# Kernel tuning notes

Measured on AMD Instinct MI355X. Metric: run time of the kernel, lower is better.

Reference implementation:

```python
import jax, jax.numpy as jnp
import numpy as np

NUM_TILES = 64
TPC = 8            # tiles per cluster
GRID = 16          # spline grid size
EPS = 1e-5


def setup_inputs() -> dict:
    key = jax.random.key(0)
    ks = jax.random.split(key, 6)
    B, S, D, T, DH, G = 2, 1024, 512, NUM_TILES, 128, GRID
    x = jax.random.normal(ks[0], (B, S, D), dtype=jnp.float32)
    gamma = jnp.ones((D,), jnp.float32)
    beta = jnp.zeros((D,), jnp.float32)
    # torch layouts: down.weight [DH, D], up.weight [D, DH]
    Wd = jax.random.normal(ks[1], (T, DH, D), dtype=jnp.float32) * 0.02
    spline_bases = jax.random.normal(ks[2], (T, DH, G), dtype=jnp.float32) * 0.1
    spline_slopes = jax.random.normal(ks[3], (T, DH, G), dtype=jnp.float32) * 0.1
    Wu = jax.random.normal(ks[4], (T, D, DH), dtype=jnp.float32) * 0.02
    scale = jnp.full((T,), 0.1, jnp.float32)
    return {"x": x, "gamma": gamma, "beta": beta, "Wd": Wd,
            "spline_bases": spline_bases, "spline_slopes": spline_slopes,
            "Wu": Wu, "scale": scale}


def reference(x, gamma, beta, Wd, spline_bases, spline_slopes, Wu, scale):
    B, S, D = x.shape
    T, DH, _ = Wd.shape
    C = T // TPC
    N = B * S

    # LayerNorm
    mu = x.mean(-1, keepdims=True)
    var = ((x - mu) ** 2).mean(-1, keepdims=True)
    xn = (x - mu) * jax.lax.rsqrt(var + EPS) * gamma + beta
    xf = xn.reshape(N, D)

    # Signatures (first call: ema == current tile signatures)
    tile_sigs = jnp.sign(Wd.mean(axis=1))                         # [T, D]
    cluster_sigs = jnp.sign(tile_sigs.reshape(C, TPC, D).mean(1))  # [C, D]

    # Hierarchical routing: cluster -> tile
    in_sigs = jnp.sign(xf)                                        # [N, D]
    best_c = jnp.argmax(in_sigs @ cluster_sigs.T, axis=-1)        # [N]
    tile_scores = (in_sigs @ tile_sigs.T).reshape(N, C, TPC)      # [N, C, TPC]
    sc = jnp.take_along_axis(tile_scores, best_c[:, None, None], axis=1)[:, 0, :]
    local_best = jnp.argmax(sc, axis=-1)                          # [N]
    tidx = best_c * TPC + local_best                              # [N]

    # Dispatch: gather per-token expert weights, down-project
    h = jnp.einsum('nd,nhd->nh', xf, Wd[tidx])                    # [N, DH]

    # Spline nonlinearity
    hn = jax.nn.sigmoid(h)
    idx = jnp.clip((hn * GRID).astype(jnp.int32), 0, GRID - 1)    # [N, DH]
    base = jnp.take_along_axis(spline_bases[tidx], idx[..., None], axis=-1)[..., 0]
    slope = jnp.take_along_axis(spline_slopes[tidx], idx[..., None], axis=-1)[..., 0]
    local_pos = hn * GRID - idx.astype(h.dtype)                   # (hn - idx*cell)/cell
    hs = base + slope * local_pos                                 # [N, DH]

    # Up-project, per-tile scale, combine (dropout is identity in eval)
    y = jnp.einsum('nh,ndh->nd', hs, Wu[tidx]) * scale[tidx][:, None]
    return x + y.reshape(B, S, D)
```

## Files before the change

### kernel.cpp

```cpp
#include <hip/hip_runtime.h>
#include <hip/hip_bf16.h>
#include <math.h>

#define NTILES 64
#define TPC 8
#define NCLUST 8
#define GRID_SZ 16
#define DIM 512
#define DHID 128
#define NTOK 2048
#define LN_EPS 1e-5f
#define TB 16
#define NCHUNK_MAX 192

typedef __attribute__((ext_vector_type(8))) short bf16x8;
typedef __attribute__((ext_vector_type(4))) float f32x4;
typedef unsigned long long u64;

static __device__ __forceinline__ unsigned short bf16bits(float f) {
    union { __hip_bfloat16 h; unsigned short s; } u;
    u.h = __float2bfloat16(f);
    return u.s;
}

static __device__ __forceinline__ bf16x8 cvt8v(float4 a, float4 b) {
    float e[8] = {a.x, a.y, a.z, a.w, b.x, b.y, b.z, b.w};
    bf16x8 v;
    #pragma unroll
    for (int i = 0; i < 8; ++i) v[i] = (short)bf16bits(e[i]);
    return v;
}

static __device__ __forceinline__ bf16x8 cvt8(const float* p) {
    return cvt8v(*(const float4*)p, *(const float4*)(p + 4));
}

static __device__ __forceinline__ u64 maj3(u64 a, u64 b, u64 c) {
    return (a & b) | (c & (a ^ b));
}

static __device__ __forceinline__ bool route_chunk(const int* counts, int lane, int cb,
                                                   int& t, int& base, int& m) {
    int cnt_l = counts[lane];
    int nck = (cnt_l + TB - 1) / TB;
    int pre = nck;
    #pragma unroll
    for (int off = 1; off < 64; off <<= 1) {
        int u = __shfl_up(pre, off);
        if (lane >= off) pre += u;
    }
    int total = __shfl(pre, 63);
    pre -= nck;
    if (cb >= total) return false;
    u64 msk = __ballot(cb >= pre && cb < pre + nck);
    t = (int)__builtin_ctzll(msk);
    base = (cb - __shfl(pre, t)) * TB;
    m = min(TB, __shfl(cnt_l, t) - base);
    return true;
}

__global__ __launch_bounds__(512) void k_prep(const float* __restrict__ x,
                                              const float* __restrict__ gamma,
                                              const float* __restrict__ beta,
                                              const float* __restrict__ Wd,
                                              unsigned short* __restrict__ wd_b,
                                              unsigned short* __restrict__ xn_b,
                                              u64* __restrict__ tbits,
                                              int* __restrict__ counts) {
    int bid = blockIdx.x;
    int tid = threadIdx.x;
    int lane = tid & 63;
    int wv = tid >> 6;
    if (bid < NTILES) {
        int t = bid;
        if (bid == 0 && tid < NTILES) counts[tid] = 0;
        const float* bp = Wd + (size_t)t * DHID * DIM + tid;
        unsigned short* bb = wd_b + (size_t)t * DHID * DIM + tid;
        float s0 = 0.f, s1 = 0.f, s2 = 0.f, s3 = 0.f;
        #pragma unroll 4
        for (int j = 0; j < DHID; j += 4) {
            float v0 = bp[(size_t)(j + 0) * DIM];
            float v1 = bp[(size_t)(j + 1) * DIM];
            float v2 = bp[(size_t)(j + 2) * DIM];
            float v3 = bp[(size_t)(j + 3) * DIM];
            bb[(size_t)(j + 0) * DIM] = bf16bits(v0);
            bb[(size_t)(j + 1) * DIM] = bf16bits(v1);
            bb[(size_t)(j + 2) * DIM] = bf16bits(v2);
            bb[(size_t)(j + 3) * DIM] = bf16bits(v3);
            s0 += v0; s1 += v1; s2 += v2; s3 += v3;
        }
        float s = (s0 + s1) + (s2 + s3);
        u64 b = __ballot(s < 0.f);
        if (lane == 0) tbits[t * 8 + wv] = b;
    } else {
        int n = (bid - NTILES) * 8 + wv;
        const float* xr = x + (size_t)n * DIM;
        float v[8];
        float sum = 0.f;
        #pragma unroll
        for (int j = 0; j < 8; ++j) { float t = xr[lane + 64 * j]; v[j] = t; sum += t; }
        #pragma unroll
        for (int off = 32; off; off >>= 1) sum += __shfl_xor(sum, off);
        float mu = sum * (1.f / DIM);
        float sq = 0.f;
        #pragma unroll
        for (int j = 0; j < 8; ++j) { float t = v[j] - mu; sq += t * t; }
        #pragma unroll
        for (int off = 32; off; off >>= 1) sq += __shfl_xor(sq, off);
        float rs = rsqrtf(sq * (1.f / DIM) + LN_EPS);
        #pragma unroll
        for (int j = 0; j < 8; ++j) {
            int d = lane + 64 * j;
            float xv = (v[j] - mu) * rs * gamma[d] + beta[d];
            xn_b[(size_t)n * DIM + d] = bf16bits(xv);
        }
    }
}

__global__ __launch_bounds__(256) void k_route(const unsigned short* __restrict__ xn_b,
                                               const u64* __restrict__ tbits,
                                               int* __restrict__ counts,
                                               int* __restrict__ list) {
    int n = blockIdx.x * 4 + (threadIdx.x >> 6);
    int lane = threadIdx.x & 63;
    u64 xb[8];
    #pragma unroll
    for (int j = 0; j < 8; ++j) {
        unsigned short u = xn_b[(size_t)n * DIM + lane + 64 * j];
        xb[j] = __ballot((u & 0x8000u) != 0 && (u & 0x7fffu) != 0);
    }
    const u64* tb = tbits + lane * 8;
    int ts = 0;
    #pragma unroll
    for (int j = 0; j < 8; ++j) ts += __popcll(xb[j] ^ tb[j]);
    int tscore = DIM - 2 * ts;

    int c = lane >> 3, jw = lane & 7;
    u64 x0 = tbits[(c * TPC + 0) * 8 + jw], x1 = tbits[(c * TPC + 1) * 8 + jw];
    u64 x2 = tbits[(c * TPC + 2) * 8 + jw], x3 = tbits[(c * TPC + 3) * 8 + jw];
    u64 x4 = tbits[(c * TPC + 4) * 8 + jw], x5 = tbits[(c * TPC + 5) * 8 + jw];
    u64 x6 = tbits[(c * TPC + 6) * 8 + jw], x7 = tbits[(c * TPC + 7) * 8 + jw];
    u64 s0 = x0 ^ x1 ^ x2, c0 = maj3(x0, x1, x2);
    u64 s1 = x3 ^ x4 ^ x5, c1 = maj3(x3, x4, x5);
    u64 s2 = x6 ^ x7,      c2 = x6 & x7;
    u64 t0 = s0 ^ s1 ^ s2, t1 = maj3(s0, s1, s2);
    u64 p = c0 ^ c1, q = c0 & c1;
    u64 r = c2 ^ t1, s_ = c2 & t1;
    u64 S0 = p ^ r, car = p & r;
    u64 W0 = (q ^ s_) ^ car;
    u64 W1 = (q & s_) | (car & (q ^ s_));
    u64 cbit = W1 | (W0 & (S0 | t0));
    u64 cmsk = ~(W0 & ~W1 & ~S0 & ~t0);
    int ps = __popcll(cmsk) - 2 * __popcll((xb[jw] ^ cbit) & cmsk);
    ps += __shfl_xor(ps, 1);
    ps += __shfl_xor(ps, 2);
    ps += __shfl_xor(ps, 4);

    int bc = 0, best = __shfl(ps, 0);
    #pragma unroll
    for (int k = 1; k < NCLUST; ++k) {
        int v = __shfl(ps, k * 8);
        if (v > best) { best = v; bc = k; }
    }
    int bt = bc * TPC, bts = __shfl(tscore, bc * TPC);
    #pragma unroll
    for (int k = 1; k < TPC; ++k) {
        int v = __shfl(tscore, bc * TPC + k);
        if (v > bts) { bts = v; bt = bc * TPC + k; }
    }
    if (lane == 0) {
        int slot = atomicAdd(&counts[bt], 1);
        list[(size_t)bt * NTOK + slot] = n;
    }
}

__global__ __launch_bounds__(512, 2) void k_ffn(const float* __restrict__ x,
                                                const unsigned short* __restrict__ xn_b,
                                                const unsigned short* __restrict__ wd_b,
                                                const float* __restrict__ sb,
                                                const float* __restrict__ ss,
                                                const float* __restrict__ Wu,
                                                const float* __restrict__ scale,
                                                const int* __restrict__ counts,
                                                const int* __restrict__ list,
                                                float* __restrict__ out) {
    int tid = threadIdx.x;
    int lane = tid & 63;
    int wv = tid >> 6;
    int cb = ((int)blockIdx.x & 7) * (NCHUNK_MAX / 8) + ((int)blockIdx.x >> 3);
    int t, base, m;
    if (!route_chunk(counts, lane, cb, t, base, m)) return;

    __shared__ __align__(16) unsigned short hsl[TB * DHID];

    int mrow = lane & 15;
    int ko = (lane >> 4) * 8;
    int tokm = list[(size_t)t * NTOK + base + min(mrow, m - 1)];

    const unsigned short* xr = xn_b + (size_t)tokm * DIM;
    const unsigned short* wr = wd_b + ((size_t)t * DHID + wv * 16 + mrow) * DIM;
    f32x4 acc0 = {0.f, 0.f, 0.f, 0.f}, acc1 = acc0;
    #pragma unroll
    for (int kk = 0; kk < 8; ++kk) {
        int d0 = kk * 32 + ko;
        int d1 = (kk + 8) * 32 + ko;
        bf16x8 a0 = *(const bf16x8*)(xr + d0);
        bf16x8 b0 = *(const bf16x8*)(wr + d0);
        acc0 = __builtin_amdgcn_mfma_f32_16x16x32_bf16(a0, b0, acc0, 0, 0, 0);
        bf16x8 a1 = *(const bf16x8*)(xr + d1);
        bf16x8 b1 = *(const bf16x8*)(wr + d1);
        acc1 = __builtin_amdgcn_mfma_f32_16x16x32_bf16(a1, b1, acc1, 0, 0, 0);
    }
    f32x4 acc = acc0 + acc1;

    const float* wru0 = Wu + ((size_t)t * DIM + wv * 64 + mrow) * DHID;
    float4 pfa[4], pfb[4];
    #pragma unroll
    for (int kk = 0; kk < 4; ++kk) {
        pfa[kk] = *(const float4*)(wru0 + kk * 32 + ko);
        pfb[kk] = *(const float4*)(wru0 + kk * 32 + ko + 4);
    }

    int dh = wv * 16 + mrow;
    const float* sbt = sb + ((size_t)t * DHID + dh) * GRID_SZ;
    const float* sst = ss + ((size_t)t * DHID + dh) * GRID_SZ;
    #pragma unroll
    for (int r = 0; r < 4; ++r) {
        int tr = (lane >> 4) * 4 + r;
        float h = acc[r];
        float hn = 1.f / (1.f + expf(-h));
        float g = hn * (float)GRID_SZ;
        int idx = (int)g;
        idx = idx > GRID_SZ - 1 ? GRID_SZ - 1 : idx;
        float lp = g - (float)idx;
        float val = sbt[idx] + sst[idx] * lp;
        hsl[(tr * DHID + dh) ^ ((tr & 7) << 3)] = bf16bits(val);
    }
    __syncthreads();

    float sc_t = scale[t];
    bf16x8 a2[4];
    #pragma unroll
    for (int kk = 0; kk < 4; ++kk)
        a2[kk] = *(const bf16x8*)&hsl[(mrow * DHID + kk * 32 + ko) ^ ((mrow & 7) << 3)];
    #pragma unroll
    for (int nt = 0; nt < 4; ++nt) {
        int d = wv * 64 + nt * 16 + mrow;
        const float* wru = Wu + ((size_t)t * DIM + d) * DHID;
        f32x4 au = {0.f, 0.f, 0.f, 0.f};
        #pragma unroll
        for (int kk = 0; kk < 4; ++kk) {
            bf16x8 b = (nt == 0) ? cvt8v(pfa[kk], pfb[kk])
                                 : cvt8(wru + kk * 32 + ko);
            au = __builtin_amdgcn_mfma_f32_16x16x32_bf16(a2[kk], b, au, 0, 0, 0);
        }
        #pragma unroll
        for (int r = 0; r < 4; ++r) {
            int tr = (lane >> 4) * 4 + r;
            int tok_tr = __shfl(tokm, tr);
            if (tr < m) {
                size_t o = (size_t)tok_tr * DIM + d;
                out[o] = x[o] + au[r] * sc_t;
            }
        }
    }
}

extern "C" void kernel_launch(void* const* d_in, const int* in_sizes, int n_in,
                              void* d_out, int out_size, void* d_ws, size_t ws_size,
                              hipStream_t stream) {
    const float* x     = (const float*)d_in[0];
    const float* gamma = (const float*)d_in[1];
    const float* beta  = (const float*)d_in[2];
    const float* Wd    = (const float*)d_in[3];
    const float* sb    = (const float*)d_in[4];
    const float* ss    = (const float*)d_in[5];
    const float* Wu    = (const float*)d_in[6];
    const float* scale = (const float*)d_in[7];
    float* out = (float*)d_out;

    u64*   tbits         = (u64*)d_ws;
    int*   counts        = (int*)(tbits + NTILES * 8);
    int*   list          = counts + NTILES;
    unsigned short* xn_b = (unsigned short*)(list + (size_t)NTILES * NTOK);
    unsigned short* wd_b = xn_b + (size_t)NTOK * DIM;

    k_prep<<<NTILES + NTOK / 8, 512, 0, stream>>>(x, gamma, beta, Wd, wd_b, xn_b, tbits, counts);
    k_route<<<NTOK / 4, 256, 0, stream>>>(xn_b, tbits, counts, list);
    k_ffn<<<NCHUNK_MAX, 512, 0, stream>>>(x, xn_b, wd_b, sb, ss, Wu, scale, counts, list, out);
}
```

Measured before the change: 50.49 us.

## Pre-convert Wu to bf16 in prep kernel and prefetch all FFN operands into registers

The prep kernel gains 256 extra blocks that convert Wu to bf16 in workspace, and the Wd conversion now uses float4 loads with a shared-memory reduction for the sign sums. The FFN kernel loads all down-projection operands and all bf16 up-projection weights into registers up front instead of interleaving loads with MFMAs and converting fp32 Wu per chunk. This halves Wu bytes read in the FFN and removes repeated per-chunk conversion. In exchange, the prep kernel writes a full bf16 copy of Wu, and register pressure rises, so launch bounds drop to one block per CU.

```diff
diff --git a/kernel.cpp b/kernel.cpp
--- a/kernel.cpp
+++ b/kernel.cpp
@@ -14,6 +14,7 @@
 #define NCHUNK_MAX 192
 
 typedef __attribute__((ext_vector_type(8))) short bf16x8;
+typedef __attribute__((ext_vector_type(4))) unsigned short u16x4;
 typedef __attribute__((ext_vector_type(4))) float f32x4;
 typedef unsigned long long u64;
 
@@ -23,16 +24,14 @@
     return u.s;
 }
 
-static __device__ __forceinline__ bf16x8 cvt8v(float4 a, float4 b) {
+static __device__ __forceinline__ bf16x8 cvt8(const float* p) {
+    float4 a = *(const float4*)p;
+    float4 b = *(const float4*)(p + 4);
     float e[8] = {a.x, a.y, a.z, a.w, b.x, b.y, b.z, b.w};
     bf16x8 v;
     #pragma unroll
     for (int i = 0; i < 8; ++i) v[i] = (short)bf16bits(e[i]);
     return v;
-}
-
-static __device__ __forceinline__ bf16x8 cvt8(const float* p) {
-    return cvt8v(*(const float4*)p, *(const float4*)(p + 4));
 }
 
 static __device__ __forceinline__ u64 maj3(u64 a, u64 b, u64 c) {
@@ -63,7 +62,9 @@
                                               const float* __restrict__ gamma,
                                               const float* __restrict__ beta,
                                               const float* __restrict__ Wd,
+                                              const float* __restrict__ Wu,
                                               unsigned short* __restrict__ wd_b,
+                                              unsigned short* __restrict__ wu_b,
                                               unsigned short* __restrict__ xn_b,
                                               u64* __restrict__ tbits,
                                               int* __restrict__ counts) {
@@ -74,25 +75,25 @@
     if (bid < NTILES) {
         int t = bid;
         if (bid == 0 && tid < NTILES) counts[tid] = 0;
-        const float* bp = Wd + (size_t)t * DHID * DIM + tid;
-        unsigned short* bb = wd_b + (size_t)t * DHID * DIM + tid;
-        float s0 = 0.f, s1 = 0.f, s2 = 0.f, s3 = 0.f;
-        #pragma unroll 4
-        for (int j = 0; j < DHID; j += 4) {
-            float v0 = bp[(size_t)(j + 0) * DIM];
-            float v1 = bp[(size_t)(j + 1) * DIM];
-            float v2 = bp[(size_t)(j + 2) * DIM];
-            float v3 = bp[(size_t)(j + 3) * DIM];
-            bb[(size_t)(j + 0) * DIM] = bf16bits(v0);
-            bb[(size_t)(j + 1) * DIM] = bf16bits(v1);
-            bb[(size_t)(j + 2) * DIM] = bf16bits(v2);
-            bb[(size_t)(j + 3) * DIM] = bf16bits(v3);
-            s0 += v0; s1 += v1; s2 += v2; s3 += v3;
-        }
-        float s = (s0 + s1) + (s2 + s3);
+        int q = tid >> 7;
+        int c4 = tid & 127;
+        const float* wp = Wd + ((size_t)t * DHID + q * 32) * DIM + c4 * 4;
+        unsigned short* bp = wd_b + ((size_t)t * DHID + q * 32) * DIM + c4 * 4;
+        float4 a = {0.f, 0.f, 0.f, 0.f};
+        #pragma unroll
+        for (int j = 0; j < 32; ++j) {
+            float4 v = *(const float4*)(wp + (size_t)j * DIM);
+            u16x4 h = {bf16bits(v.x), bf16bits(v.y), bf16bits(v.z), bf16bits(v.w)};
+            *(u16x4*)(bp + (size_t)j * DIM) = h;
+            a.x += v.x; a.y += v.y; a.z += v.z; a.w += v.w;
+        }
+        __shared__ float ps[4][DIM];
+        *(float4*)&ps[q][c4 * 4] = a;
+        __syncthreads();
+        float s = ps[0][tid] + ps[1][tid] + ps[2][tid] + ps[3][tid];
         u64 b = __ballot(s < 0.f);
         if (lane == 0) tbits[t * 8 + wv] = b;
-    } else {
+    } else if (bid < 320) {
         int n = (bid - NTILES) * 8 + wv;
         const float* xr = x + (size_t)n * DIM;
         float v[8];
@@ -113,6 +114,13 @@
             int d = lane + 64 * j;
             float xv = (v[j] - mu) * rs * gamma[d] + beta[d];
             xn_b[(size_t)n * DIM + d] = bf16bits(xv);
+        }
+    } else {
+        size_t basei = (size_t)(bid - 320) * 16384;
+        #pragma unroll
+        for (int k = 0; k < 4; ++k) {
+            size_t off = basei + (size_t)tid * 8 + (size_t)k * 4096;
+            *(bf16x8*)(wu_b + off) = cvt8(Wu + off);
         }
     }
 }
@@ -151,15 +159,15 @@
     u64 W1 = (q & s_) | (car & (q ^ s_));
     u64 cbit = W1 | (W0 & (S0 | t0));
     u64 cmsk = ~(W0 & ~W1 & ~S0 & ~t0);
-    int ps = __popcll(cmsk) - 2 * __popcll((xb[jw] ^ cbit) & cmsk);
-    ps += __shfl_xor(ps, 1);
-    ps += __shfl_xor(ps, 2);
-    ps += __shfl_xor(ps, 4);
-
-    int bc = 0, best = __shfl(ps, 0);
+    int psc = __popcll(cmsk) - 2 * __popcll((xb[jw] ^ cbit) & cmsk);
+    psc += __shfl_xor(psc, 1);
+    psc += __shfl_xor(psc, 2);
+    psc += __shfl_xor(psc, 4);
+
+    int bc = 0, best = __shfl(psc, 0);
     #pragma unroll
     for (int k = 1; k < NCLUST; ++k) {
-        int v = __shfl(ps, k * 8);
+        int v = __shfl(psc, k * 8);
         if (v > best) { best = v; bc = k; }
     }
     int bt = bc * TPC, bts = __shfl(tscore, bc * TPC);
@@ -174,12 +182,12 @@
     }
 }
 
-__global__ __launch_bounds__(512, 2) void k_ffn(const float* __restrict__ x,
+__global__ __launch_bounds__(512, 1) void k_ffn(const float* __restrict__ x,
                                                 const unsigned short* __restrict__ xn_b,
                                                 const unsigned short* __restrict__ wd_b,
                                                 const float* __restrict__ sb,
                                                 const float* __restrict__ ss,
-                                                const float* __restrict__ Wu,
+                                                const unsigned short* __restrict__ wu_b,
                                                 const float* __restrict__ scale,
                                                 const int* __restrict__ counts,
                                                 const int* __restrict__ list,
@@ -199,26 +207,28 @@
 
     const unsigned short* xr = xn_b + (size_t)tokm * DIM;
     const unsigned short* wr = wd_b + ((size_t)t * DHID + wv * 16 + mrow) * DIM;
+    bf16x8 wreg[16], areg[16];
+    #pragma unroll
+    for (int kk = 0; kk < 16; ++kk) {
+        int d = kk * 32 + ko;
+        wreg[kk] = *(const bf16x8*)(wr + d);
+        areg[kk] = *(const bf16x8*)(xr + d);
+    }
     f32x4 acc0 = {0.f, 0.f, 0.f, 0.f}, acc1 = acc0;
     #pragma unroll
     for (int kk = 0; kk < 8; ++kk) {
-        int d0 = kk * 32 + ko;
-        int d1 = (kk + 8) * 32 + ko;
-        bf16x8 a0 = *(const bf16x8*)(xr + d0);
-        bf16x8 b0 = *(const bf16x8*)(wr + d0);
-        acc0 = __builtin_amdgcn_mfma_f32_16x16x32_bf16(a0, b0, acc0, 0, 0, 0);
-        bf16x8 a1 = *(const bf16x8*)(xr + d1);
-        bf16x8 b1 = *(const bf16x8*)(wr + d1);
-        acc1 = __builtin_amdgcn_mfma_f32_16x16x32_bf16(a1, b1, acc1, 0, 0, 0);
+        acc0 = __builtin_amdgcn_mfma_f32_16x16x32_bf16(areg[2 * kk], wreg[2 * kk], acc0, 0, 0, 0);
+        acc1 = __builtin_amdgcn_mfma_f32_16x16x32_bf16(areg[2 * kk + 1], wreg[2 * kk + 1], acc1, 0, 0, 0);
     }
     f32x4 acc = acc0 + acc1;
 
-    const float* wru0 = Wu + ((size_t)t * DIM + wv * 64 + mrow) * DHID;
-    float4 pfa[4], pfb[4];
-    #pragma unroll
-    for (int kk = 0; kk < 4; ++kk) {
-        pfa[kk] = *(const float4*)(wru0 + kk * 32 + ko);
-        pfb[kk] = *(const float4*)(wru0 + kk * 32 + ko + 4);
+    bf16x8 wupf[16];
+    #pragma unroll
+    for (int nt = 0; nt < 4; ++nt) {
+        const unsigned short* wru = wu_b + ((size_t)t * DIM + wv * 64 + nt * 16 + mrow) * DHID;
+        #pragma unroll
+        for (int kk = 0; kk < 4; ++kk)
+            wupf[nt * 4 + kk] = *(const bf16x8*)(wru + kk * 32 + ko);
     }
 
     int dh = wv * 16 + mrow;
@@ -246,14 +256,10 @@
     #pragma unroll
     for (int nt = 0; nt < 4; ++nt) {
         int d = wv * 64 + nt * 16 + mrow;
-        const float* wru = Wu + ((size_t)t * DIM + d) * DHID;
         f32x4 au = {0.f, 0.f, 0.f, 0.f};
         #pragma unroll
-        for (int kk = 0; kk < 4; ++kk) {
-            bf16x8 b = (nt == 0) ? cvt8v(pfa[kk], pfb[kk])
-                                 : cvt8(wru + kk * 32 + ko);
-            au = __builtin_amdgcn_mfma_f32_16x16x32_bf16(a2[kk], b, au, 0, 0, 0);
-        }
+        for (int kk = 0; kk < 4; ++kk)
+            au = __builtin_amdgcn_mfma_f32_16x16x32_bf16(a2[kk], wupf[nt * 4 + kk], au, 0, 0, 0);
         #pragma unroll
         for (int r = 0; r < 4; ++r) {
             int tr = (lane >> 4) * 4 + r;
@@ -284,8 +290,9 @@
     int*   list          = counts + NTILES;
     unsigned short* xn_b = (unsigned short*)(list + (size_t)NTILES * NTOK);
     unsigned short* wd_b = xn_b + (size_t)NTOK * DIM;
-
-    k_prep<<<NTILES + NTOK / 8, 512, 0, stream>>>(x, gamma, beta, Wd, wd_b, xn_b, tbits, counts);
+    unsigned short* wu_b = wd_b + (size_t)NTILES * DHID * DIM;
+
+    k_prep<<<576, 512, 0, stream>>>(x, gamma, beta, Wd, Wu, wd_b, wu_b, xn_b, tbits, counts);
     k_route<<<NTOK / 4, 256, 0, stream>>>(xn_b, tbits, counts, list);
-    k_ffn<<<NCHUNK_MAX, 512, 0, stream>>>(x, xn_b, wd_b, sb, ss, Wu, scale, counts, list, out);
-}
+    k_ffn<<<NCHUNK_MAX, 512, 0, stream>>>(x, xn_b, wd_b, sb, ss, wu_b, scale, counts, list, out);
+}
```

Result: faster. 45.51 us (-9.9%).
